# Performance work log

Hardware: AMD Instinct MI355X
Metric: run time of the kernel (lower is better)

## Reference

```python
import jax, jax.numpy as jnp
import numpy as np

N_NODES = 10000
N_EDGES = 320000
N_GRAPHS = 64
IN_DIM = 1
HID = 256


def setup_inputs() -> dict:
    key = jax.random.key(0)
    ks = jax.random.split(key, 12)
    s = 1.0 / np.sqrt(HID)
    inp = {
        "x": jax.random.normal(ks[0], (N_NODES, IN_DIM), dtype=jnp.float32),
        "edge_index": jax.random.randint(ks[1], (2, N_EDGES), 0, N_NODES, dtype=jnp.int64),
        "batch": jnp.sort(jax.random.randint(ks[2], (N_NODES,), 0, N_GRAPHS, dtype=jnp.int64)),
        "W_emb": jax.random.normal(ks[3], (IN_DIM, HID), dtype=jnp.float32),
        "b_emb": jnp.zeros((HID,), dtype=jnp.float32),
        "W1a": jax.random.normal(ks[4], (HID, HID), dtype=jnp.float32) * s,
        "b1a": jnp.zeros((HID,), dtype=jnp.float32),
        "W1b": jax.random.normal(ks[5], (HID, HID), dtype=jnp.float32) * s,
        "b1b": jnp.zeros((HID,), dtype=jnp.float32),
        "W2a": jax.random.normal(ks[6], (HID, HID), dtype=jnp.float32) * s,
        "b2a": jnp.zeros((HID,), dtype=jnp.float32),
        "W2b": jax.random.normal(ks[7], (HID, HID), dtype=jnp.float32) * s,
        "b2b": jnp.zeros((HID,), dtype=jnp.float32),
    }
    return inp


def _pointnet_conv(h, src, dst, Wa, ba, Wb, bb):
    # gather x_j -> 2-layer MLP per edge -> scatter-max at dst (PyG aggr='max')
    msg = jax.nn.relu(h[src] @ Wa + ba) @ Wb + bb          # [E, HID]
    agg = jax.ops.segment_max(msg, dst, num_segments=N_NODES)
    # PyG fills nodes with no incoming messages with 0
    return jnp.where(jnp.isneginf(agg), 0.0, agg)


def reference(x, edge_index, batch, W_emb, b_emb, W1a, b1a, W1b, b1b, W2a, b2a, W2b, b2b):
    src, dst = edge_index[0], edge_index[1]
    h = jax.nn.silu(x @ W_emb + b_emb)                     # [N, HID]
    h = h + jax.nn.silu(_pointnet_conv(h, src, dst, W1a, b1a, W1b, b1b))
    h = h + jax.nn.silu(_pointnet_conv(h, src, dst, W2a, b2a, W2b, b2b))
    # global_mean_pool over graphs
    sums = jax.ops.segment_sum(h, batch, num_segments=N_GRAPHS)          # [G, HID]
    cnts = jax.ops.segment_sum(jnp.ones((h.shape[0],), h.dtype), batch, num_segments=N_GRAPHS)
    return sums / jnp.maximum(cnts, 1.0)[:, None]
```

## Files before the change

kernel.cpp:

```cpp
#include <hip/hip_runtime.h>
#include <hip/hip_bf16.h>
#include <math.h>

#define HID 256
#define CAP 128
#define FB 64

typedef __attribute__((ext_vector_type(8))) short bf16x8;
typedef __attribute__((ext_vector_type(8))) unsigned short u16x8;
typedef __attribute__((ext_vector_type(4))) float f32x4;

__device__ __forceinline__ float silu_f(float z) {
    return z / (1.0f + __expf(-z));
}
__device__ __forceinline__ unsigned short f2bf(float f) {
    unsigned int u = __float_as_uint(f);
    u = (u + 0x7FFFu + ((u >> 16) & 1u)) >> 16;
    return (unsigned short)u;
}
__device__ __forceinline__ float bf2f(unsigned short b) {
    return __uint_as_float(((unsigned int)b) << 16);
}
__device__ __forceinline__ void max8(float m[8], u16x8 v) {
#pragma unroll
    for (int k = 0; k < 8; ++k) m[k] = fmaxf(m[k], bf2f(v[k]));
}

__global__ __launch_bounds__(256) void k_prep(
    const float* __restrict__ w0, const float* __restrict__ w1,
    const float* __restrict__ w2, const float* __restrict__ w3,
    unsigned short* __restrict__ o0, unsigned short* __restrict__ o1,
    unsigned short* __restrict__ o2, unsigned short* __restrict__ o3,
    const int* __restrict__ dst, int* __restrict__ cbase,
    const int* __restrict__ batch, int* __restrict__ goff,
    int N, int G, int E, int chunk) {
    __shared__ __align__(16) int shp[10000];
    int b = blockIdx.x;
    int tid = threadIdx.x;
    if (b < 64) {
        float (*ls)[65] = (float(*)[65])shp;
        int mat = b >> 4;
        int tile = b & 15;
        int k0 = (tile >> 2) * 64;
        int n0 = (tile & 3) * 64;
        const float* in = (mat == 0) ? w0 : (mat == 1) ? w1 : (mat == 2) ? w2 : w3;
        unsigned short* op = (mat == 0) ? o0 : (mat == 1) ? o1 : (mat == 2) ? o2 : o3;
        int lrb = tid >> 4;
        int lc = (tid & 15) * 4;
#pragma unroll
        for (int p = 0; p < 4; ++p) {
            int lr = p * 16 + lrb;
            float4 v = *(const float4*)(in + (size_t)(k0 + lr) * HID + n0 + lc);
            ls[lr][lc + 0] = v.x; ls[lr][lc + 1] = v.y;
            ls[lr][lc + 2] = v.z; ls[lr][lc + 3] = v.w;
        }
        __syncthreads();
#pragma unroll
        for (int p = 0; p < 4; ++p) {
            int ln = p * 16 + lrb;
            ushort4 q;
            q.x = f2bf(ls[lc + 0][ln]);
            q.y = f2bf(ls[lc + 1][ln]);
            q.z = f2bf(ls[lc + 2][ln]);
            q.w = f2bf(ls[lc + 3][ln]);
            *(ushort4*)(op + (size_t)(n0 + ln) * HID + k0 + lc) = q;
        }
    } else if (b == 64) {
        int g = tid;
        if (g > G) return;
        int lo = 0, hi = N;
        while (lo < hi) {
            int mid = (lo + hi) >> 1;
            if (batch[mid] < g) lo = mid + 1; else hi = mid;
        }
        goff[g] = lo;
    } else {
        int fb = b - 65;
        int* hist = shp;
        for (int i = tid; i < N; i += 256) hist[i] = 0;
        __syncthreads();
        int e0 = fb * chunk;
        int e1 = min(E, e0 + chunk);
        for (int e = e0 + tid * 4; e + 3 < e1; e += 1024) {
            int4 d4 = *(const int4*)(dst + e);
            atomicAdd(&hist[d4.x], 1);
            atomicAdd(&hist[d4.y], 1);
            atomicAdd(&hist[d4.z], 1);
            atomicAdd(&hist[d4.w], 1);
        }
        int rem = (e1 - e0) & 3;
        if (tid < rem) atomicAdd(&hist[dst[e1 - rem + tid]], 1);
        __syncthreads();
        for (int i = tid; i < N; i += 256) cbase[(size_t)fb * N + i] = hist[i];
    }
}

__global__ __launch_bounds__(256) void k_prefix(int* __restrict__ cbase,
                                                int* __restrict__ cnt, int N) {
    int d = blockIdx.x * 256 + threadIdx.x;
    if (d >= N) return;
    int run = 0;
#pragma unroll
    for (int b = 0; b < FB; ++b) {
        int c = cbase[(size_t)b * N + d];
        cbase[(size_t)b * N + d] = run;
        run += c;
    }
    cnt[d] = run;
}

__global__ __launch_bounds__(256) void k_mlp1f(
    const float* __restrict__ x, const float* __restrict__ Wemb,
    const float* __restrict__ bemb,
    const unsigned short* __restrict__ Wta, const float* __restrict__ ba,
    const unsigned short* __restrict__ Wtb, const float* __restrict__ bbv,
    unsigned short* __restrict__ hb, unsigned short* __restrict__ t2,
    const int* __restrict__ src, const int* __restrict__ dst,
    const int* __restrict__ cbase, unsigned short* __restrict__ csr,
    int M, int E, int MT, int chunk) {
    __shared__ __align__(16) int shbuf[10000];
    unsigned short (*As)[264]  = (unsigned short(*)[264])shbuf;
    unsigned short (*t1s)[264] = (unsigned short(*)[264])((char*)shbuf + 16896);
    int b = blockIdx.x;
    int tid = threadIdx.x;

    if (b >= MT) {
        int fb = b - MT;
        int* hist = shbuf;
        for (int i = tid; i < M; i += 256) hist[i] = 0;
        __syncthreads();
        int e0 = fb * chunk;
        int e1 = min(E, e0 + chunk);
        const int* cb = cbase + (size_t)fb * M;
        for (int e = e0 + tid * 4; e + 3 < e1; e += 1024) {
            int4 d4 = *(const int4*)(dst + e);
            int4 s4 = *(const int4*)(src + e);
            int r0 = atomicAdd(&hist[d4.x], 1);
            int r1 = atomicAdd(&hist[d4.y], 1);
            int r2 = atomicAdd(&hist[d4.z], 1);
            int r3 = atomicAdd(&hist[d4.w], 1);
            int p0 = cb[d4.x] + r0;
            int p1 = cb[d4.y] + r1;
            int p2 = cb[d4.z] + r2;
            int p3 = cb[d4.w] + r3;
            if (p0 < CAP) csr[d4.x * CAP + p0] = (unsigned short)s4.x;
            if (p1 < CAP) csr[d4.y * CAP + p1] = (unsigned short)s4.y;
            if (p2 < CAP) csr[d4.z * CAP + p2] = (unsigned short)s4.z;
            if (p3 < CAP) csr[d4.w * CAP + p3] = (unsigned short)s4.w;
        }
        int rem = (e1 - e0) & 3;
        if (tid < rem) {
            int e = e1 - rem + tid;
            int d = dst[e];
            int r = atomicAdd(&hist[d], 1);
            int p = cb[d] + r;
            if (p < CAP) csr[d * CAP + p] = (unsigned short)src[e];
        }
        return;
    }

    int lane = tid & 63;
    int wave = tid >> 6;
    int quad = lane >> 4;
    int r = lane & 15;
    int m0 = b * 32;
    int colw = wave * 64;

    {
        int row = tid >> 3;
        int c0 = (tid & 7) * 32;
        int grow = m0 + row;
        float xv = (grow < M) ? x[grow] : 0.0f;
#pragma unroll
        for (int j = 0; j < 8; ++j) {
            int c = c0 + j * 4;
            ushort4 q;
            q.x = f2bf(silu_f(xv * Wemb[c + 0] + bemb[c + 0]));
            q.y = f2bf(silu_f(xv * Wemb[c + 1] + bemb[c + 1]));
            q.z = f2bf(silu_f(xv * Wemb[c + 2] + bemb[c + 2]));
            q.w = f2bf(silu_f(xv * Wemb[c + 3] + bemb[c + 3]));
            if (grow < M) *(ushort4*)(hb + (size_t)grow * HID + c) = q;
            *(ushort4*)&As[row][c] = q;
        }
        __syncthreads();
    }

    f32x4 acc[2][4];
#pragma unroll
    for (int rt = 0; rt < 2; ++rt)
#pragma unroll
        for (int nt = 0; nt < 4; ++nt) acc[rt][nt] = (f32x4)0.0f;
#pragma unroll
    for (int ks = 0; ks < 8; ++ks) {
        bf16x8 a0 = *(const bf16x8*)&As[r][ks * 32 + quad * 8];
        bf16x8 a1 = *(const bf16x8*)&As[r + 16][ks * 32 + quad * 8];
#pragma unroll
        for (int nt = 0; nt < 4; ++nt) {
            bf16x8 bfr = *(const bf16x8*)(Wta + (size_t)(colw + nt * 16 + r) * HID
                                          + ks * 32 + quad * 8);
            acc[0][nt] = __builtin_amdgcn_mfma_f32_16x16x32_bf16(a0, bfr, acc[0][nt], 0, 0, 0);
            acc[1][nt] = __builtin_amdgcn_mfma_f32_16x16x32_bf16(a1, bfr, acc[1][nt], 0, 0, 0);
        }
    }
#pragma unroll
    for (int nt = 0; nt < 4; ++nt) {
        int col = colw + nt * 16 + r;
        float bv = ba[col];
#pragma unroll
        for (int rt = 0; rt < 2; ++rt)
#pragma unroll
            for (int i = 0; i < 4; ++i) {
                float v = fmaxf(acc[rt][nt][i] + bv, 0.0f);
                t1s[rt * 16 + quad * 4 + i][col] = f2bf(v);
            }
    }
    __syncthreads();

    f32x4 acc2[2][4];
#pragma unroll
    for (int rt = 0; rt < 2; ++rt)
#pragma unroll
        for (int nt = 0; nt < 4; ++nt) acc2[rt][nt] = (f32x4)0.0f;
#pragma unroll
    for (int ks = 0; ks < 8; ++ks) {
        bf16x8 a0 = *(const bf16x8*)&t1s[r][ks * 32 + quad * 8];
        bf16x8 a1 = *(const bf16x8*)&t1s[r + 16][ks * 32 + quad * 8];
#pragma unroll
        for (int nt = 0; nt < 4; ++nt) {
            bf16x8 bfr = *(const bf16x8*)(Wtb + (size_t)(colw + nt * 16 + r) * HID
                                          + ks * 32 + quad * 8);
            acc2[0][nt] = __builtin_amdgcn_mfma_f32_16x16x32_bf16(a0, bfr, acc2[0][nt], 0, 0, 0);
            acc2[1][nt] = __builtin_amdgcn_mfma_f32_16x16x32_bf16(a1, bfr, acc2[1][nt], 0, 0, 0);
        }
    }
#pragma unroll
    for (int nt = 0; nt < 4; ++nt) {
        int col = colw + nt * 16 + r;
        float bv = bbv[col];
#pragma unroll
        for (int rt = 0; rt < 2; ++rt)
#pragma unroll
            for (int i = 0; i < 4; ++i) {
                int row = m0 + rt * 16 + quad * 4 + i;
                if (row < M) t2[(size_t)row * HID + col] = f2bf(acc2[rt][nt][i] + bv);
            }
    }
}

__global__ __launch_bounds__(256) void k_mlp2(
    const unsigned short* __restrict__ Aglob,
    const unsigned short* __restrict__ Wta, const float* __restrict__ ba,
    const unsigned short* __restrict__ Wtb, const float* __restrict__ bbv,
    unsigned short* __restrict__ t2, int M) {
    __shared__ unsigned short t1s[32][264];
    int tid = threadIdx.x;
    int lane = tid & 63;
    int wave = tid >> 6;
    int quad = lane >> 4;
    int r = lane & 15;
    int m0 = blockIdx.x * 32;
    int colw = wave * 64;

    f32x4 acc[2][4];
#pragma unroll
    for (int rt = 0; rt < 2; ++rt)
#pragma unroll
        for (int nt = 0; nt < 4; ++nt) acc[rt][nt] = (f32x4)0.0f;

    int ar0 = m0 + r;        if (ar0 >= M) ar0 = M - 1;
    int ar1 = m0 + 16 + r;   if (ar1 >= M) ar1 = M - 1;

#pragma unroll
    for (int ks = 0; ks < 8; ++ks) {
        bf16x8 a0 = *(const bf16x8*)(Aglob + (size_t)ar0 * HID + ks * 32 + quad * 8);
        bf16x8 a1 = *(const bf16x8*)(Aglob + (size_t)ar1 * HID + ks * 32 + quad * 8);
#pragma unroll
        for (int nt = 0; nt < 4; ++nt) {
            bf16x8 bfr = *(const bf16x8*)(Wta + (size_t)(colw + nt * 16 + r) * HID
                                          + ks * 32 + quad * 8);
            acc[0][nt] = __builtin_amdgcn_mfma_f32_16x16x32_bf16(a0, bfr, acc[0][nt], 0, 0, 0);
            acc[1][nt] = __builtin_amdgcn_mfma_f32_16x16x32_bf16(a1, bfr, acc[1][nt], 0, 0, 0);
        }
    }
#pragma unroll
    for (int nt = 0; nt < 4; ++nt) {
        int col = colw + nt * 16 + r;
        float bv = ba[col];
#pragma unroll
        for (int rt = 0; rt < 2; ++rt)
#pragma unroll
            for (int i = 0; i < 4; ++i) {
                float v = fmaxf(acc[rt][nt][i] + bv, 0.0f);
                t1s[rt * 16 + quad * 4 + i][col] = f2bf(v);
            }
    }
    __syncthreads();

    f32x4 acc2[2][4];
#pragma unroll
    for (int rt = 0; rt < 2; ++rt)
#pragma unroll
        for (int nt = 0; nt < 4; ++nt) acc2[rt][nt] = (f32x4)0.0f;
#pragma unroll
    for (int ks = 0; ks < 8; ++ks) {
        bf16x8 a0 = *(const bf16x8*)&t1s[r][ks * 32 + quad * 8];
        bf16x8 a1 = *(const bf16x8*)&t1s[r + 16][ks * 32 + quad * 8];
#pragma unroll
        for (int nt = 0; nt < 4; ++nt) {
            bf16x8 bfr = *(const bf16x8*)(Wtb + (size_t)(colw + nt * 16 + r) * HID
                                          + ks * 32 + quad * 8);
            acc2[0][nt] = __builtin_amdgcn_mfma_f32_16x16x32_bf16(a0, bfr, acc2[0][nt], 0, 0, 0);
            acc2[1][nt] = __builtin_amdgcn_mfma_f32_16x16x32_bf16(a1, bfr, acc2[1][nt], 0, 0, 0);
        }
    }
#pragma unroll
    for (int nt = 0; nt < 4; ++nt) {
        int col = colw + nt * 16 + r;
        float bv = bbv[col];
#pragma unroll
        for (int rt = 0; rt < 2; ++rt)
#pragma unroll
            for (int i = 0; i < 4; ++i) {
                int row = m0 + rt * 16 + quad * 4 + i;
                if (row < M) t2[(size_t)row * HID + col] = f2bf(acc2[rt][nt][i] + bv);
            }
    }
}

__global__ __launch_bounds__(256) void k_agg(const unsigned short* __restrict__ t2,
                                             const int* __restrict__ cnt,
                                             const unsigned short* __restrict__ csr,
                                             unsigned short* __restrict__ hb, int N) {
    int lane = threadIdx.x & 63;
    int node = (blockIdx.x * blockDim.x + threadIdx.x) >> 6;
    if (node >= N) return;
    int half = lane >> 5;
    int lc = (lane & 31) * 8;
    const unsigned short* base = t2 + lc;

    int deg = cnt[node];
    if (deg > CAP) deg = CAP;
    const unsigned short* rowp = csr + (size_t)node * CAP;
    size_t o = (size_t)node * HID + lc;
    u16x8 hq = *(const u16x8*)(hb + o);

    float m[8];
#pragma unroll
    for (int k = 0; k < 8; ++k) m[k] = -INFINITY;

    int i = 0;
    for (; i + 16 <= deg; i += 16) {
        int s[8];
#pragma unroll
        for (int j = 0; j < 8; ++j) s[j] = rowp[i + 2 * j + half];
        u16x8 v[8];
#pragma unroll
        for (int j = 0; j < 8; ++j) v[j] = *(const u16x8*)(base + (size_t)s[j] * HID);
#pragma unroll
        for (int j = 0; j < 8; ++j) max8(m, v[j]);
    }
    if (i + 8 <= deg) {
        int s[4];
#pragma unroll
        for (int j = 0; j < 4; ++j) s[j] = rowp[i + 2 * j + half];
        u16x8 v[4];
#pragma unroll
        for (int j = 0; j < 4; ++j) v[j] = *(const u16x8*)(base + (size_t)s[j] * HID);
#pragma unroll
        for (int j = 0; j < 4; ++j) max8(m, v[j]);
        i += 8;
    }
    for (; i < deg; i += 2) {
        int idx = i + half; if (idx >= deg) idx = deg - 1;
        int s = rowp[idx];
        u16x8 v = *(const u16x8*)(base + (size_t)s * HID);
        max8(m, v);
    }

#pragma unroll
    for (int k = 0; k < 8; ++k) m[k] = fmaxf(m[k], __shfl_xor(m[k], 32, 64));
    if (deg == 0) {
#pragma unroll
        for (int k = 0; k < 8; ++k) m[k] = 0.0f;
    }

    if (half == 0) {
        u16x8 q;
#pragma unroll
        for (int k = 0; k < 8; ++k) q[k] = f2bf(bf2f(hq[k]) + silu_f(m[k]));
        *(u16x8*)(hb + o) = q;
    }
}

__global__ __launch_bounds__(1024) void k_pool(const unsigned short* __restrict__ hb,
                                               const int* __restrict__ goff,
                                               float* __restrict__ out) {
    __shared__ float part[3][HID];
    int g = blockIdx.x;
    int tid = threadIdx.x;
    int c = tid & 255;
    int chunk = tid >> 8;
    int beg = goff[g], end = goff[g + 1];
    float s = 0.f;
    for (int n = beg + chunk; n < end; n += 4) s += bf2f(hb[(size_t)n * HID + c]);
    if (chunk > 0) part[chunk - 1][c] = s;
    __syncthreads();
    if (chunk == 0) {
        s += part[0][c] + part[1][c] + part[2][c];
        int cnt = end - beg;
        out[g * HID + c] = s / (float)(cnt > 0 ? cnt : 1);
    }
}

extern "C" void kernel_launch(void* const* d_in, const int* in_sizes, int n_in,
                              void* d_out, int out_size, void* d_ws, size_t ws_size,
                              hipStream_t stream) {
    const float* x     = (const float*)d_in[0];
    const int*   ei    = (const int*)d_in[1];
    const int*   batch = (const int*)d_in[2];
    const float* Wemb  = (const float*)d_in[3];
    const float* bemb  = (const float*)d_in[4];
    const float* W1a   = (const float*)d_in[5];
    const float* b1a   = (const float*)d_in[6];
    const float* W1b   = (const float*)d_in[7];
    const float* b1b   = (const float*)d_in[8];
    const float* W2a   = (const float*)d_in[9];
    const float* b2a   = (const float*)d_in[10];
    const float* W2b   = (const float*)d_in[11];
    const float* b2b   = (const float*)d_in[12];
    float* out = (float*)d_out;

    const int N = in_sizes[0];
    const int E = in_sizes[1] / 2;
    const int G = out_size / HID;
    const int* src = ei;
    const int* dst = ei + E;

    char* ws = (char*)d_ws;
    unsigned short* hb   = (unsigned short*)ws; ws += (size_t)N * HID * 2;
    unsigned short* t2   = (unsigned short*)ws; ws += (size_t)N * HID * 2;
    unsigned short* Wt1a = (unsigned short*)ws; ws += (size_t)HID * HID * 2;
    unsigned short* Wt1b = (unsigned short*)ws; ws += (size_t)HID * HID * 2;
    unsigned short* Wt2a = (unsigned short*)ws; ws += (size_t)HID * HID * 2;
    unsigned short* Wt2b = (unsigned short*)ws; ws += (size_t)HID * HID * 2;
    int* cnt   = (int*)ws; ws += (size_t)N * 4;
    int* goff  = (int*)ws; ws += (size_t)(G + 1) * 4;
    int* cbase = (int*)ws; ws += (size_t)FB * N * 4;
    unsigned short* csr = (unsigned short*)ws; ws += (size_t)N * CAP * 2;

    const int chunk = (((E + FB - 1) / FB) + 3) & ~3;
    const int MT = (N + 31) / 32;

    k_prep<<<64 + 1 + FB, 256, 0, stream>>>(W1a, W1b, W2a, W2b,
                                            Wt1a, Wt1b, Wt2a, Wt2b,
                                            dst, cbase, batch, goff, N, G, E, chunk);

    k_prefix<<<(N + 255) / 256, 256, 0, stream>>>(cbase, cnt, N);

    k_mlp1f<<<MT + FB, 256, 0, stream>>>(x, Wemb, bemb, Wt1a, b1a, Wt1b, b1b,
                                         hb, t2, src, dst, cbase, csr, N, E, MT, chunk);

    int agg_blocks = (N * 64 + 255) / 256;

    k_agg<<<agg_blocks, 256, 0, stream>>>(t2, cnt, csr, hb, N);

    k_mlp2<<<MT, 256, 0, stream>>>(hb, Wt2a, b2a, Wt2b, b2b, t2, N);

    k_agg<<<agg_blocks, 256, 0, stream>>>(t2, cnt, csr, hb, N);

    k_pool<<<G, 1024, 0, stream>>>(hb, goff, out);
}
```

Measured before the change: 194.7 us.

## Fuse all stages into one persistent cooperative kernel with grid syncs

Replaces the seven separate kernel launches (prep, prefix, mlp1, agg, mlp2, agg, pool) with one cooperative persistent kernel. Stages are separated by grid-wide barriers and each stage loops over its work items with a grid stride. The grid is sized from the occupancy query, capped at four blocks per CU across 256 CUs. The aggregation tail is also changed to a single padded 8-wide gather with clamped indices. This is meant to remove launch gaps and inter-kernel drain, at the cost of grid-sync overhead and a fixed grid that may load-balance worse in the GEMM and gather stages.

```diff
diff --git a/kernel.cpp b/kernel.cpp
--- a/kernel.cpp
+++ b/kernel.cpp
@@ -1,10 +1,13 @@
 #include <hip/hip_runtime.h>
+#include <hip/hip_cooperative_groups.h>
 #include <hip/hip_bf16.h>
 #include <math.h>
 
 #define HID 256
 #define CAP 128
 #define FB 64
+
+namespace cg = cooperative_groups;
 
 typedef __attribute__((ext_vector_type(8))) short bf16x8;
 typedef __attribute__((ext_vector_type(8))) unsigned short u16x8;
@@ -26,314 +29,11 @@
     for (int k = 0; k < 8; ++k) m[k] = fmaxf(m[k], bf2f(v[k]));
 }
 
-__global__ __launch_bounds__(256) void k_prep(
-    const float* __restrict__ w0, const float* __restrict__ w1,
-    const float* __restrict__ w2, const float* __restrict__ w3,
-    unsigned short* __restrict__ o0, unsigned short* __restrict__ o1,
-    unsigned short* __restrict__ o2, unsigned short* __restrict__ o3,
-    const int* __restrict__ dst, int* __restrict__ cbase,
-    const int* __restrict__ batch, int* __restrict__ goff,
-    int N, int G, int E, int chunk) {
-    __shared__ __align__(16) int shp[10000];
-    int b = blockIdx.x;
-    int tid = threadIdx.x;
-    if (b < 64) {
-        float (*ls)[65] = (float(*)[65])shp;
-        int mat = b >> 4;
-        int tile = b & 15;
-        int k0 = (tile >> 2) * 64;
-        int n0 = (tile & 3) * 64;
-        const float* in = (mat == 0) ? w0 : (mat == 1) ? w1 : (mat == 2) ? w2 : w3;
-        unsigned short* op = (mat == 0) ? o0 : (mat == 1) ? o1 : (mat == 2) ? o2 : o3;
-        int lrb = tid >> 4;
-        int lc = (tid & 15) * 4;
-#pragma unroll
-        for (int p = 0; p < 4; ++p) {
-            int lr = p * 16 + lrb;
-            float4 v = *(const float4*)(in + (size_t)(k0 + lr) * HID + n0 + lc);
-            ls[lr][lc + 0] = v.x; ls[lr][lc + 1] = v.y;
-            ls[lr][lc + 2] = v.z; ls[lr][lc + 3] = v.w;
-        }
-        __syncthreads();
-#pragma unroll
-        for (int p = 0; p < 4; ++p) {
-            int ln = p * 16 + lrb;
-            ushort4 q;
-            q.x = f2bf(ls[lc + 0][ln]);
-            q.y = f2bf(ls[lc + 1][ln]);
-            q.z = f2bf(ls[lc + 2][ln]);
-            q.w = f2bf(ls[lc + 3][ln]);
-            *(ushort4*)(op + (size_t)(n0 + ln) * HID + k0 + lc) = q;
-        }
-    } else if (b == 64) {
-        int g = tid;
-        if (g > G) return;
-        int lo = 0, hi = N;
-        while (lo < hi) {
-            int mid = (lo + hi) >> 1;
-            if (batch[mid] < g) lo = mid + 1; else hi = mid;
-        }
-        goff[g] = lo;
-    } else {
-        int fb = b - 65;
-        int* hist = shp;
-        for (int i = tid; i < N; i += 256) hist[i] = 0;
-        __syncthreads();
-        int e0 = fb * chunk;
-        int e1 = min(E, e0 + chunk);
-        for (int e = e0 + tid * 4; e + 3 < e1; e += 1024) {
-            int4 d4 = *(const int4*)(dst + e);
-            atomicAdd(&hist[d4.x], 1);
-            atomicAdd(&hist[d4.y], 1);
-            atomicAdd(&hist[d4.z], 1);
-            atomicAdd(&hist[d4.w], 1);
-        }
-        int rem = (e1 - e0) & 3;
-        if (tid < rem) atomicAdd(&hist[dst[e1 - rem + tid]], 1);
-        __syncthreads();
-        for (int i = tid; i < N; i += 256) cbase[(size_t)fb * N + i] = hist[i];
-    }
-}
-
-__global__ __launch_bounds__(256) void k_prefix(int* __restrict__ cbase,
-                                                int* __restrict__ cnt, int N) {
-    int d = blockIdx.x * 256 + threadIdx.x;
-    if (d >= N) return;
-    int run = 0;
-#pragma unroll
-    for (int b = 0; b < FB; ++b) {
-        int c = cbase[(size_t)b * N + d];
-        cbase[(size_t)b * N + d] = run;
-        run += c;
-    }
-    cnt[d] = run;
-}
-
-__global__ __launch_bounds__(256) void k_mlp1f(
-    const float* __restrict__ x, const float* __restrict__ Wemb,
-    const float* __restrict__ bemb,
-    const unsigned short* __restrict__ Wta, const float* __restrict__ ba,
-    const unsigned short* __restrict__ Wtb, const float* __restrict__ bbv,
-    unsigned short* __restrict__ hb, unsigned short* __restrict__ t2,
-    const int* __restrict__ src, const int* __restrict__ dst,
-    const int* __restrict__ cbase, unsigned short* __restrict__ csr,
-    int M, int E, int MT, int chunk) {
-    __shared__ __align__(16) int shbuf[10000];
-    unsigned short (*As)[264]  = (unsigned short(*)[264])shbuf;
-    unsigned short (*t1s)[264] = (unsigned short(*)[264])((char*)shbuf + 16896);
-    int b = blockIdx.x;
-    int tid = threadIdx.x;
-
-    if (b >= MT) {
-        int fb = b - MT;
-        int* hist = shbuf;
-        for (int i = tid; i < M; i += 256) hist[i] = 0;
-        __syncthreads();
-        int e0 = fb * chunk;
-        int e1 = min(E, e0 + chunk);
-        const int* cb = cbase + (size_t)fb * M;
-        for (int e = e0 + tid * 4; e + 3 < e1; e += 1024) {
-            int4 d4 = *(const int4*)(dst + e);
-            int4 s4 = *(const int4*)(src + e);
-            int r0 = atomicAdd(&hist[d4.x], 1);
-            int r1 = atomicAdd(&hist[d4.y], 1);
-            int r2 = atomicAdd(&hist[d4.z], 1);
-            int r3 = atomicAdd(&hist[d4.w], 1);
-            int p0 = cb[d4.x] + r0;
-            int p1 = cb[d4.y] + r1;
-            int p2 = cb[d4.z] + r2;
-            int p3 = cb[d4.w] + r3;
-            if (p0 < CAP) csr[d4.x * CAP + p0] = (unsigned short)s4.x;
-            if (p1 < CAP) csr[d4.y * CAP + p1] = (unsigned short)s4.y;
-            if (p2 < CAP) csr[d4.z * CAP + p2] = (unsigned short)s4.z;
-            if (p3 < CAP) csr[d4.w * CAP + p3] = (unsigned short)s4.w;
-        }
-        int rem = (e1 - e0) & 3;
-        if (tid < rem) {
-            int e = e1 - rem + tid;
-            int d = dst[e];
-            int r = atomicAdd(&hist[d], 1);
-            int p = cb[d] + r;
-            if (p < CAP) csr[d * CAP + p] = (unsigned short)src[e];
-        }
-        return;
-    }
-
-    int lane = tid & 63;
-    int wave = tid >> 6;
-    int quad = lane >> 4;
-    int r = lane & 15;
-    int m0 = b * 32;
-    int colw = wave * 64;
-
-    {
-        int row = tid >> 3;
-        int c0 = (tid & 7) * 32;
-        int grow = m0 + row;
-        float xv = (grow < M) ? x[grow] : 0.0f;
-#pragma unroll
-        for (int j = 0; j < 8; ++j) {
-            int c = c0 + j * 4;
-            ushort4 q;
-            q.x = f2bf(silu_f(xv * Wemb[c + 0] + bemb[c + 0]));
-            q.y = f2bf(silu_f(xv * Wemb[c + 1] + bemb[c + 1]));
-            q.z = f2bf(silu_f(xv * Wemb[c + 2] + bemb[c + 2]));
-            q.w = f2bf(silu_f(xv * Wemb[c + 3] + bemb[c + 3]));
-            if (grow < M) *(ushort4*)(hb + (size_t)grow * HID + c) = q;
-            *(ushort4*)&As[row][c] = q;
-        }
-        __syncthreads();
-    }
-
-    f32x4 acc[2][4];
-#pragma unroll
-    for (int rt = 0; rt < 2; ++rt)
-#pragma unroll
-        for (int nt = 0; nt < 4; ++nt) acc[rt][nt] = (f32x4)0.0f;
-#pragma unroll
-    for (int ks = 0; ks < 8; ++ks) {
-        bf16x8 a0 = *(const bf16x8*)&As[r][ks * 32 + quad * 8];
-        bf16x8 a1 = *(const bf16x8*)&As[r + 16][ks * 32 + quad * 8];
-#pragma unroll
-        for (int nt = 0; nt < 4; ++nt) {
-            bf16x8 bfr = *(const bf16x8*)(Wta + (size_t)(colw + nt * 16 + r) * HID
-                                          + ks * 32 + quad * 8);
-            acc[0][nt] = __builtin_amdgcn_mfma_f32_16x16x32_bf16(a0, bfr, acc[0][nt], 0, 0, 0);
-            acc[1][nt] = __builtin_amdgcn_mfma_f32_16x16x32_bf16(a1, bfr, acc[1][nt], 0, 0, 0);
-        }
-    }
-#pragma unroll
-    for (int nt = 0; nt < 4; ++nt) {
-        int col = colw + nt * 16 + r;
-        float bv = ba[col];
-#pragma unroll
-        for (int rt = 0; rt < 2; ++rt)
-#pragma unroll
-            for (int i = 0; i < 4; ++i) {
-                float v = fmaxf(acc[rt][nt][i] + bv, 0.0f);
-                t1s[rt * 16 + quad * 4 + i][col] = f2bf(v);
-            }
-    }
-    __syncthreads();
-
-    f32x4 acc2[2][4];
-#pragma unroll
-    for (int rt = 0; rt < 2; ++rt)
-#pragma unroll
-        for (int nt = 0; nt < 4; ++nt) acc2[rt][nt] = (f32x4)0.0f;
-#pragma unroll
-    for (int ks = 0; ks < 8; ++ks) {
-        bf16x8 a0 = *(const bf16x8*)&t1s[r][ks * 32 + quad * 8];
-        bf16x8 a1 = *(const bf16x8*)&t1s[r + 16][ks * 32 + quad * 8];
-#pragma unroll
-        for (int nt = 0; nt < 4; ++nt) {
-            bf16x8 bfr = *(const bf16x8*)(Wtb + (size_t)(colw + nt * 16 + r) * HID
-                                          + ks * 32 + quad * 8);
-            acc2[0][nt] = __builtin_amdgcn_mfma_f32_16x16x32_bf16(a0, bfr, acc2[0][nt], 0, 0, 0);
-            acc2[1][nt] = __builtin_amdgcn_mfma_f32_16x16x32_bf16(a1, bfr, acc2[1][nt], 0, 0, 0);
-        }
-    }
-#pragma unroll
-    for (int nt = 0; nt < 4; ++nt) {
-        int col = colw + nt * 16 + r;
-        float bv = bbv[col];
-#pragma unroll
-        for (int rt = 0; rt < 2; ++rt)
-#pragma unroll
-            for (int i = 0; i < 4; ++i) {
-                int row = m0 + rt * 16 + quad * 4 + i;
-                if (row < M) t2[(size_t)row * HID + col] = f2bf(acc2[rt][nt][i] + bv);
-            }
-    }
-}
-
-__global__ __launch_bounds__(256) void k_mlp2(
-    const unsigned short* __restrict__ Aglob,
-    const unsigned short* __restrict__ Wta, const float* __restrict__ ba,
-    const unsigned short* __restrict__ Wtb, const float* __restrict__ bbv,
-    unsigned short* __restrict__ t2, int M) {
-    __shared__ unsigned short t1s[32][264];
-    int tid = threadIdx.x;
-    int lane = tid & 63;
-    int wave = tid >> 6;
-    int quad = lane >> 4;
-    int r = lane & 15;
-    int m0 = blockIdx.x * 32;
-    int colw = wave * 64;
-
-    f32x4 acc[2][4];
-#pragma unroll
-    for (int rt = 0; rt < 2; ++rt)
-#pragma unroll
-        for (int nt = 0; nt < 4; ++nt) acc[rt][nt] = (f32x4)0.0f;
-
-    int ar0 = m0 + r;        if (ar0 >= M) ar0 = M - 1;
-    int ar1 = m0 + 16 + r;   if (ar1 >= M) ar1 = M - 1;
-
-#pragma unroll
-    for (int ks = 0; ks < 8; ++ks) {
-        bf16x8 a0 = *(const bf16x8*)(Aglob + (size_t)ar0 * HID + ks * 32 + quad * 8);
-        bf16x8 a1 = *(const bf16x8*)(Aglob + (size_t)ar1 * HID + ks * 32 + quad * 8);
-#pragma unroll
-        for (int nt = 0; nt < 4; ++nt) {
-            bf16x8 bfr = *(const bf16x8*)(Wta + (size_t)(colw + nt * 16 + r) * HID
-                                          + ks * 32 + quad * 8);
-            acc[0][nt] = __builtin_amdgcn_mfma_f32_16x16x32_bf16(a0, bfr, acc[0][nt], 0, 0, 0);
-            acc[1][nt] = __builtin_amdgcn_mfma_f32_16x16x32_bf16(a1, bfr, acc[1][nt], 0, 0, 0);
-        }
-    }
-#pragma unroll
-    for (int nt = 0; nt < 4; ++nt) {
-        int col = colw + nt * 16 + r;
-        float bv = ba[col];
-#pragma unroll
-        for (int rt = 0; rt < 2; ++rt)
-#pragma unroll
-            for (int i = 0; i < 4; ++i) {
-                float v = fmaxf(acc[rt][nt][i] + bv, 0.0f);
-                t1s[rt * 16 + quad * 4 + i][col] = f2bf(v);
-            }
-    }
-    __syncthreads();
-
-    f32x4 acc2[2][4];
-#pragma unroll
-    for (int rt = 0; rt < 2; ++rt)
-#pragma unroll
-        for (int nt = 0; nt < 4; ++nt) acc2[rt][nt] = (f32x4)0.0f;
-#pragma unroll
-    for (int ks = 0; ks < 8; ++ks) {
-        bf16x8 a0 = *(const bf16x8*)&t1s[r][ks * 32 + quad * 8];
-        bf16x8 a1 = *(const bf16x8*)&t1s[r + 16][ks * 32 + quad * 8];
-#pragma unroll
-        for (int nt = 0; nt < 4; ++nt) {
-            bf16x8 bfr = *(const bf16x8*)(Wtb + (size_t)(colw + nt * 16 + r) * HID
-                                          + ks * 32 + quad * 8);
-            acc2[0][nt] = __builtin_amdgcn_mfma_f32_16x16x32_bf16(a0, bfr, acc2[0][nt], 0, 0, 0);
-            acc2[1][nt] = __builtin_amdgcn_mfma_f32_16x16x32_bf16(a1, bfr, acc2[1][nt], 0, 0, 0);
-        }
-    }
-#pragma unroll
-    for (int nt = 0; nt < 4; ++nt) {
-        int col = colw + nt * 16 + r;
-        float bv = bbv[col];
-#pragma unroll
-        for (int rt = 0; rt < 2; ++rt)
-#pragma unroll
-            for (int i = 0; i < 4; ++i) {
-                int row = m0 + rt * 16 + quad * 4 + i;
-                if (row < M) t2[(size_t)row * HID + col] = f2bf(acc2[rt][nt][i] + bv);
-            }
-    }
-}
-
-__global__ __launch_bounds__(256) void k_agg(const unsigned short* __restrict__ t2,
-                                             const int* __restrict__ cnt,
-                                             const unsigned short* __restrict__ csr,
-                                             unsigned short* __restrict__ hb, int N) {
-    int lane = threadIdx.x & 63;
-    int node = (blockIdx.x * blockDim.x + threadIdx.x) >> 6;
-    if (node >= N) return;
+__device__ __forceinline__ void agg_one(const unsigned short* __restrict__ t2,
+                                        const int* __restrict__ cnt,
+                                        const unsigned short* __restrict__ csr,
+                                        unsigned short* __restrict__ hb,
+                                        int node, int lane) {
     int half = lane >> 5;
     int lc = (lane & 31) * 8;
     const unsigned short* base = t2 + lc;
@@ -359,22 +59,18 @@
 #pragma unroll
         for (int j = 0; j < 8; ++j) max8(m, v[j]);
     }
-    if (i + 8 <= deg) {
-        int s[4];
-#pragma unroll
-        for (int j = 0; j < 4; ++j) s[j] = rowp[i + 2 * j + half];
-        u16x8 v[4];
-#pragma unroll
-        for (int j = 0; j < 4; ++j) v[j] = *(const u16x8*)(base + (size_t)s[j] * HID);
-#pragma unroll
-        for (int j = 0; j < 4; ++j) max8(m, v[j]);
-        i += 8;
-    }
-    for (; i < deg; i += 2) {
-        int idx = i + half; if (idx >= deg) idx = deg - 1;
-        int s = rowp[idx];
-        u16x8 v = *(const u16x8*)(base + (size_t)s * HID);
-        max8(m, v);
+    if (i < deg) {
+        int s[8];
+#pragma unroll
+        for (int j = 0; j < 8; ++j) {
+            int idx = i + 2 * j + half; if (idx >= deg) idx = deg - 1;
+            s[j] = rowp[idx];
+        }
+        u16x8 v[8];
+#pragma unroll
+        for (int j = 0; j < 8; ++j) v[j] = *(const u16x8*)(base + (size_t)s[j] * HID);
+#pragma unroll
+        for (int j = 0; j < 8; ++j) max8(m, v[j]);
     }
 
 #pragma unroll
@@ -383,7 +79,6 @@
 #pragma unroll
         for (int k = 0; k < 8; ++k) m[k] = 0.0f;
     }
-
     if (half == 0) {
         u16x8 q;
 #pragma unroll
@@ -392,23 +87,331 @@
     }
 }
 
-__global__ __launch_bounds__(1024) void k_pool(const unsigned short* __restrict__ hb,
-                                               const int* __restrict__ goff,
-                                               float* __restrict__ out) {
-    __shared__ float part[3][HID];
-    int g = blockIdx.x;
+__global__ __launch_bounds__(256, 4) void k_fused(
+    const float* __restrict__ x, const int* __restrict__ src,
+    const int* __restrict__ dst, const int* __restrict__ batch,
+    const float* __restrict__ Wemb, const float* __restrict__ bemb,
+    const float* __restrict__ W1a, const float* __restrict__ b1a,
+    const float* __restrict__ W1b, const float* __restrict__ b1b,
+    const float* __restrict__ W2a, const float* __restrict__ b2a,
+    const float* __restrict__ W2b, const float* __restrict__ b2b,
+    float* __restrict__ out,
+    unsigned short* __restrict__ hb, unsigned short* __restrict__ t2,
+    unsigned short* __restrict__ Wt1a, unsigned short* __restrict__ Wt1b,
+    unsigned short* __restrict__ Wt2a, unsigned short* __restrict__ Wt2b,
+    int* __restrict__ cnt, int* __restrict__ goff, int* __restrict__ cbase,
+    unsigned short* __restrict__ csr,
+    int N, int E, int G, int MT, int chunk) {
+    __shared__ __align__(16) unsigned char sh[33792];
+    cg::grid_group gg = cg::this_grid();
     int tid = threadIdx.x;
-    int c = tid & 255;
-    int chunk = tid >> 8;
-    int beg = goff[g], end = goff[g + 1];
-    float s = 0.f;
-    for (int n = beg + chunk; n < end; n += 4) s += bf2f(hb[(size_t)n * HID + c]);
-    if (chunk > 0) part[chunk - 1][c] = s;
-    __syncthreads();
-    if (chunk == 0) {
-        s += part[0][c] + part[1][c] + part[2][c];
-        int cnt = end - beg;
-        out[g * HID + c] = s / (float)(cnt > 0 ? cnt : 1);
+    int nb = gridDim.x;
+    int lane = tid & 63;
+    int wave = tid >> 6;
+    int quad = lane >> 4;
+    int r = lane & 15;
+    int colw = wave * 64;
+
+    for (int c = blockIdx.x; c < 65 + FB; c += nb) {
+        if (c < 64) {
+            float (*ls)[65] = (float(*)[65])sh;
+            int mat = c >> 4;
+            int tile = c & 15;
+            int k0 = (tile >> 2) * 64;
+            int n0 = (tile & 3) * 64;
+            const float* in = (mat == 0) ? W1a : (mat == 1) ? W1b : (mat == 2) ? W2a : W2b;
+            unsigned short* op = (mat == 0) ? Wt1a : (mat == 1) ? Wt1b : (mat == 2) ? Wt2a : Wt2b;
+            int lrb = tid >> 4;
+            int lc = (tid & 15) * 4;
+#pragma unroll
+            for (int p = 0; p < 4; ++p) {
+                int lr = p * 16 + lrb;
+                float4 v = *(const float4*)(in + (size_t)(k0 + lr) * HID + n0 + lc);
+                ls[lr][lc + 0] = v.x; ls[lr][lc + 1] = v.y;
+                ls[lr][lc + 2] = v.z; ls[lr][lc + 3] = v.w;
+            }
+            __syncthreads();
+#pragma unroll
+            for (int p = 0; p < 4; ++p) {
+                int ln = p * 16 + lrb;
+                ushort4 q;
+                q.x = f2bf(ls[lc + 0][ln]);
+                q.y = f2bf(ls[lc + 1][ln]);
+                q.z = f2bf(ls[lc + 2][ln]);
+                q.w = f2bf(ls[lc + 3][ln]);
+                *(ushort4*)(op + (size_t)(n0 + ln) * HID + k0 + lc) = q;
+            }
+        } else if (c == 64) {
+            int g = tid;
+            if (g <= G) {
+                int lo = 0, hi = N;
+                while (lo < hi) {
+                    int mid = (lo + hi) >> 1;
+                    if (batch[mid] < g) lo = mid + 1; else hi = mid;
+                }
+                goff[g] = lo;
+            }
+        } else {
+            int fb = c - 65;
+            unsigned int* hist = (unsigned int*)sh;
+            int N2 = (N + 1) >> 1;
+            for (int i = tid; i < N2; i += 256) hist[i] = 0u;
+            __syncthreads();
+            int e0 = fb * chunk;
+            int e1 = min(E, e0 + chunk);
+            for (int e = e0 + tid * 4; e + 3 < e1; e += 1024) {
+                int4 d4 = *(const int4*)(dst + e);
+                atomicAdd(&hist[d4.x >> 1], 1u << ((d4.x & 1) * 16));
+                atomicAdd(&hist[d4.y >> 1], 1u << ((d4.y & 1) * 16));
+                atomicAdd(&hist[d4.z >> 1], 1u << ((d4.z & 1) * 16));
+                atomicAdd(&hist[d4.w >> 1], 1u << ((d4.w & 1) * 16));
+            }
+            int rem = (e1 - e0) & 3;
+            if (tid < rem) {
+                int d = dst[e1 - rem + tid];
+                atomicAdd(&hist[d >> 1], 1u << ((d & 1) * 16));
+            }
+            __syncthreads();
+            for (int i = tid; i < N; i += 256)
+                cbase[(size_t)fb * N + i] =
+                    (int)((hist[i >> 1] >> ((i & 1) * 16)) & 0xffffu);
+        }
+        __syncthreads();
+    }
+    gg.sync();
+
+    for (int d = blockIdx.x * 256 + tid; d < N; d += nb * 256) {
+        int run = 0;
+#pragma unroll 8
+        for (int b = 0; b < FB; ++b) {
+            int cv = cbase[(size_t)b * N + d];
+            cbase[(size_t)b * N + d] = run;
+            run += cv;
+        }
+        cnt[d] = run;
+    }
+    gg.sync();
+
+    for (int c = blockIdx.x; c < MT + FB; c += nb) {
+        if (c >= MT) {
+            int fb = c - MT;
+            unsigned int* hist = (unsigned int*)sh;
+            int N2 = (N + 1) >> 1;
+            for (int i = tid; i < N2; i += 256) hist[i] = 0u;
+            __syncthreads();
+            int e0 = fb * chunk;
+            int e1 = min(E, e0 + chunk);
+            const int* cb = cbase + (size_t)fb * N;
+            for (int e = e0 + tid * 4; e + 3 < e1; e += 1024) {
+                int4 d4 = *(const int4*)(dst + e);
+                int4 s4 = *(const int4*)(src + e);
+                unsigned int o0 = atomicAdd(&hist[d4.x >> 1], 1u << ((d4.x & 1) * 16));
+                unsigned int o1 = atomicAdd(&hist[d4.y >> 1], 1u << ((d4.y & 1) * 16));
+                unsigned int o2 = atomicAdd(&hist[d4.z >> 1], 1u << ((d4.z & 1) * 16));
+                unsigned int o3 = atomicAdd(&hist[d4.w >> 1], 1u << ((d4.w & 1) * 16));
+                int p0 = cb[d4.x] + (int)((o0 >> ((d4.x & 1) * 16)) & 0xffffu);
+                int p1 = cb[d4.y] + (int)((o1 >> ((d4.y & 1) * 16)) & 0xffffu);
+                int p2 = cb[d4.z] + (int)((o2 >> ((d4.z & 1) * 16)) & 0xffffu);
+                int p3 = cb[d4.w] + (int)((o3 >> ((d4.w & 1) * 16)) & 0xffffu);
+                if (p0 < CAP) csr[d4.x * CAP + p0] = (unsigned short)s4.x;
+                if (p1 < CAP) csr[d4.y * CAP + p1] = (unsigned short)s4.y;
+                if (p2 < CAP) csr[d4.z * CAP + p2] = (unsigned short)s4.z;
+                if (p3 < CAP) csr[d4.w * CAP + p3] = (unsigned short)s4.w;
+            }
+            int rem = (e1 - e0) & 3;
+            if (tid < rem) {
+                int e = e1 - rem + tid;
+                int d = dst[e];
+                unsigned int ov = atomicAdd(&hist[d >> 1], 1u << ((d & 1) * 16));
+                int p = cb[d] + (int)((ov >> ((d & 1) * 16)) & 0xffffu);
+                if (p < CAP) csr[d * CAP + p] = (unsigned short)src[e];
+            }
+        } else {
+            unsigned short (*As)[264]  = (unsigned short(*)[264])sh;
+            unsigned short (*t1s)[264] = (unsigned short(*)[264])(sh + 16896);
+            int m0 = c * 32;
+            {
+                int row = tid >> 3;
+                int c0 = (tid & 7) * 32;
+                int grow = m0 + row;
+                float xv = (grow < N) ? x[grow] : 0.0f;
+#pragma unroll
+                for (int j = 0; j < 8; ++j) {
+                    int cc = c0 + j * 4;
+                    ushort4 q;
+                    q.x = f2bf(silu_f(xv * Wemb[cc + 0] + bemb[cc + 0]));
+                    q.y = f2bf(silu_f(xv * Wemb[cc + 1] + bemb[cc + 1]));
+                    q.z = f2bf(silu_f(xv * Wemb[cc + 2] + bemb[cc + 2]));
+                    q.w = f2bf(silu_f(xv * Wemb[cc + 3] + bemb[cc + 3]));
+                    if (grow < N) *(ushort4*)(hb + (size_t)grow * HID + cc) = q;
+                    *(ushort4*)&As[row][cc] = q;
+                }
+                __syncthreads();
+            }
+            f32x4 acc[2][4];
+#pragma unroll
+            for (int rt = 0; rt < 2; ++rt)
+#pragma unroll
+                for (int nt = 0; nt < 4; ++nt) acc[rt][nt] = (f32x4)0.0f;
+#pragma unroll
+            for (int ks = 0; ks < 8; ++ks) {
+                bf16x8 a0 = *(const bf16x8*)&As[r][ks * 32 + quad * 8];
+                bf16x8 a1 = *(const bf16x8*)&As[r + 16][ks * 32 + quad * 8];
+#pragma unroll
+                for (int nt = 0; nt < 4; ++nt) {
+                    bf16x8 bfr = *(const bf16x8*)(Wt1a + (size_t)(colw + nt * 16 + r) * HID
+                                                  + ks * 32 + quad * 8);
+                    acc[0][nt] = __builtin_amdgcn_mfma_f32_16x16x32_bf16(a0, bfr, acc[0][nt], 0, 0, 0);
+                    acc[1][nt] = __builtin_amdgcn_mfma_f32_16x16x32_bf16(a1, bfr, acc[1][nt], 0, 0, 0);
+                }
+            }
+#pragma unroll
+            for (int nt = 0; nt < 4; ++nt) {
+                int col = colw + nt * 16 + r;
+                float bv = b1a[col];
+#pragma unroll
+                for (int rt = 0; rt < 2; ++rt)
+#pragma unroll
+                    for (int i = 0; i < 4; ++i) {
+                        float v = fmaxf(acc[rt][nt][i] + bv, 0.0f);
+                        t1s[rt * 16 + quad * 4 + i][col] = f2bf(v);
+                    }
+            }
+            __syncthreads();
+            f32x4 acc2[2][4];
+#pragma unroll
+            for (int rt = 0; rt < 2; ++rt)
+#pragma unroll
+                for (int nt = 0; nt < 4; ++nt) acc2[rt][nt] = (f32x4)0.0f;
+#pragma unroll
+            for (int ks = 0; ks < 8; ++ks) {
+                bf16x8 a0 = *(const bf16x8*)&t1s[r][ks * 32 + quad * 8];
+                bf16x8 a1 = *(const bf16x8*)&t1s[r + 16][ks * 32 + quad * 8];
+#pragma unroll
+                for (int nt = 0; nt < 4; ++nt) {
+                    bf16x8 bfr = *(const bf16x8*)(Wt1b + (size_t)(colw + nt * 16 + r) * HID
+                                                  + ks * 32 + quad * 8);
+                    acc2[0][nt] = __builtin_amdgcn_mfma_f32_16x16x32_bf16(a0, bfr, acc2[0][nt], 0, 0, 0);
+                    acc2[1][nt] = __builtin_amdgcn_mfma_f32_16x16x32_bf16(a1, bfr, acc2[1][nt], 0, 0, 0);
+                }
+            }
+#pragma unroll
+            for (int nt = 0; nt < 4; ++nt) {
+                int col = colw + nt * 16 + r;
+                float bv = b1b[col];
+#pragma unroll
+                for (int rt = 0; rt < 2; ++rt)
+#pragma unroll
+                    for (int i = 0; i < 4; ++i) {
+                        int row = m0 + rt * 16 + quad * 4 + i;
+                        if (row < N) t2[(size_t)row * HID + col] = f2bf(acc2[rt][nt][i] + bv);
+                    }
+            }
+        }
+        __syncthreads();
+    }
+    gg.sync();
+
+    {
+        int NC = (N + 3) >> 2;
+        for (int c = blockIdx.x; c < NC; c += nb) {
+            int node = c * 4 + wave;
+            if (node < N) agg_one(t2, cnt, csr, hb, node, lane);
+        }
+    }
+    gg.sync();
+
+    for (int c = blockIdx.x; c < MT; c += nb) {
+        unsigned short (*t1s)[264] = (unsigned short(*)[264])(sh + 16896);
+        int m0 = c * 32;
+        f32x4 acc[2][4];
+#pragma unroll
+        for (int rt = 0; rt < 2; ++rt)
+#pragma unroll
+            for (int nt = 0; nt < 4; ++nt) acc[rt][nt] = (f32x4)0.0f;
+        int ar0 = m0 + r;        if (ar0 >= N) ar0 = N - 1;
+        int ar1 = m0 + 16 + r;   if (ar1 >= N) ar1 = N - 1;
+#pragma unroll
+        for (int ks = 0; ks < 8; ++ks) {
+            bf16x8 a0 = *(const bf16x8*)(hb + (size_t)ar0 * HID + ks * 32 + quad * 8);
+            bf16x8 a1 = *(const bf16x8*)(hb + (size_t)ar1 * HID + ks * 32 + quad * 8);
+#pragma unroll
+            for (int nt = 0; nt < 4; ++nt) {
+                bf16x8 bfr = *(const bf16x8*)(Wt2a + (size_t)(colw + nt * 16 + r) * HID
+                                              + ks * 32 + quad * 8);
+                acc[0][nt] = __builtin_amdgcn_mfma_f32_16x16x32_bf16(a0, bfr, acc[0][nt], 0, 0, 0);
+                acc[1][nt] = __builtin_amdgcn_mfma_f32_16x16x32_bf16(a1, bfr, acc[1][nt], 0, 0, 0);
+            }
+        }
+#pragma unroll
+        for (int nt = 0; nt < 4; ++nt) {
+            int col = colw + nt * 16 + r;
+            float bv = b2a[col];
+#pragma unroll
+            for (int rt = 0; rt < 2; ++rt)
+#pragma unroll
+                for (int i = 0; i < 4; ++i) {
+                    float v = fmaxf(acc[rt][nt][i] + bv, 0.0f);
+                    t1s[rt * 16 + quad * 4 + i][col] = f2bf(v);
+                }
+        }
+        __syncthreads();
+        f32x4 acc2[2][4];
+#pragma unroll
+        for (int rt = 0; rt < 2; ++rt)
+#pragma unroll
+            for (int nt = 0; nt < 4; ++nt) acc2[rt][nt] = (f32x4)0.0f;
+#pragma unroll
+        for (int ks = 0; ks < 8; ++ks) {
+            bf16x8 a0 = *(const bf16x8*)&t1s[r][ks * 32 + quad * 8];
+            bf16x8 a1 = *(const bf16x8*)&t1s[r + 16][ks * 32 + quad * 8];
+#pragma unroll
+            for (int nt = 0; nt < 4; ++nt) {
+                bf16x8 bfr = *(const bf16x8*)(Wt2b + (size_t)(colw + nt * 16 + r) * HID
+                                              + ks * 32 + quad * 8);
+                acc2[0][nt] = __builtin_amdgcn_mfma_f32_16x16x32_bf16(a0, bfr, acc2[0][nt], 0, 0, 0);
+                acc2[1][nt] = __builtin_amdgcn_mfma_f32_16x16x32_bf16(a1, bfr, acc2[1][nt], 0, 0, 0);
+            }
+        }
+#pragma unroll
+        for (int nt = 0; nt < 4; ++nt) {
+            int col = colw + nt * 16 + r;
+            float bv = b2b[col];
+#pragma unroll
+            for (int rt = 0; rt < 2; ++rt)
+#pragma unroll
+                for (int i = 0; i < 4; ++i) {
+                    int row = m0 + rt * 16 + quad * 4 + i;
+                    if (row < N) t2[(size_t)row * HID + col] = f2bf(acc2[rt][nt][i] + bv);
+                }
+        }
+        __syncthreads();
+    }
+    gg.sync();
+
+    {
+        int NC = (N + 3) >> 2;
+        for (int c = blockIdx.x; c < NC; c += nb) {
+            int node = c * 4 + wave;
+            if (node < N) agg_one(t2, cnt, csr, hb, node, lane);
+        }
+    }
+    gg.sync();
+
+    for (int g = blockIdx.x; g < G; g += nb) {
+        int beg = goff[g], end = goff[g + 1];
+        float s0 = 0.f, s1 = 0.f, s2 = 0.f, s3 = 0.f;
+        int n = beg;
+        for (; n + 3 < end; n += 4) {
+            s0 += bf2f(hb[(size_t)(n + 0) * HID + tid]);
+            s1 += bf2f(hb[(size_t)(n + 1) * HID + tid]);
+            s2 += bf2f(hb[(size_t)(n + 2) * HID + tid]);
+            s3 += bf2f(hb[(size_t)(n + 3) * HID + tid]);
+        }
+        for (; n < end; ++n) s0 += bf2f(hb[(size_t)n * HID + tid]);
+        float s = (s0 + s1) + (s2 + s3);
+        int cn = end - beg;
+        out[g * HID + tid] = s / (float)(cn > 0 ? cn : 1);
     }
 }
 
@@ -430,9 +433,9 @@
     const float* b2b   = (const float*)d_in[12];
     float* out = (float*)d_out;
 
-    const int N = in_sizes[0];
-    const int E = in_sizes[1] / 2;
-    const int G = out_size / HID;
+    int N = in_sizes[0];
+    int E = in_sizes[1] / 2;
+    int G = out_size / HID;
     const int* src = ei;
     const int* dst = ei + E;
 
@@ -448,25 +451,28 @@
     int* cbase = (int*)ws; ws += (size_t)FB * N * 4;
     unsigned short* csr = (unsigned short*)ws; ws += (size_t)N * CAP * 2;
 
-    const int chunk = (((E + FB - 1) / FB) + 3) & ~3;
-    const int MT = (N + 31) / 32;
-
-    k_prep<<<64 + 1 + FB, 256, 0, stream>>>(W1a, W1b, W2a, W2b,
-                                            Wt1a, Wt1b, Wt2a, Wt2b,
-                                            dst, cbase, batch, goff, N, G, E, chunk);
-
-    k_prefix<<<(N + 255) / 256, 256, 0, stream>>>(cbase, cnt, N);
-
-    k_mlp1f<<<MT + FB, 256, 0, stream>>>(x, Wemb, bemb, Wt1a, b1a, Wt1b, b1b,
-                                         hb, t2, src, dst, cbase, csr, N, E, MT, chunk);
-
-    int agg_blocks = (N * 64 + 255) / 256;
-
-    k_agg<<<agg_blocks, 256, 0, stream>>>(t2, cnt, csr, hb, N);
-
-    k_mlp2<<<MT, 256, 0, stream>>>(hb, Wt2a, b2a, Wt2b, b2b, t2, N);
-
-    k_agg<<<agg_blocks, 256, 0, stream>>>(t2, cnt, csr, hb, N);
-
-    k_pool<<<G, 1024, 0, stream>>>(hb, goff, out);
-}
+    int chunk = (((E + FB - 1) / FB) + 3) & ~3;
+    int MT = (N + 31) / 32;
+
+    static int gridBlocks = 0;
+    if (gridBlocks == 0) {
+        int perCU = 0;
+        if (hipOccupancyMaxActiveBlocksPerMultiprocessor(
+                &perCU, (const void*)k_fused, 256, 0) != hipSuccess || perCU <= 0)
+            perCU = 2;
+        if (perCU > 4) perCU = 4;
+        gridBlocks = perCU * 256;
+    }
+
+    void* kargs[] = {
+        (void*)&x, (void*)&src, (void*)&dst, (void*)&batch,
+        (void*)&Wemb, (void*)&bemb, (void*)&W1a, (void*)&b1a,
+        (void*)&W1b, (void*)&b1b, (void*)&W2a, (void*)&b2a,
+        (void*)&W2b, (void*)&b2b, (void*)&out,
+        (void*)&hb, (void*)&t2, (void*)&Wt1a, (void*)&Wt1b,
+        (void*)&Wt2a, (void*)&Wt2b, (void*)&cnt, (void*)&goff,
+        (void*)&cbase, (void*)&csr,
+        (void*)&N, (void*)&E, (void*)&G, (void*)&MT, (void*)&chunk};
+    hipLaunchCooperativeKernel((void*)k_fused, dim3(gridBlocks), dim3(256),
+                               kargs, 0, stream);
+}
```

Result: slower. 560.0 us (+187.6%).
